# Kernel optimization log

Hardware: AMD Instinct MI355X
Metric: run time of the kernel (lower is better)

Reference implementation:

```python
import jax, jax.numpy as jnp
from jax import lax
import numpy as np

# Mamba2 config from PixelMamba.__init__
D_MODEL = 128; D_STATE = 256; D_CONV = 4; EXPAND = 4; HEADDIM = 32
D_INNER = EXPAND * D_MODEL              # 512
NHEADS = D_INNER // HEADDIM             # 16
NGROUPS = 1
D_XBC = D_INNER + 2 * NGROUPS * D_STATE # 1024 (conv channels)
D_IN_PROJ = 2 * D_INNER + 2 * NGROUPS * D_STATE + NHEADS  # 1552
CHUNK = 128                             # SSD chunk length


def setup_inputs() -> dict:
    key = jax.random.key(0)
    ks = jax.random.split(key, 10)
    Bb, C, H, W = 2, 3, 64, 64
    f32 = jnp.float32
    rn = lambda k, shape, s: jax.random.normal(k, shape, f32) * s
    return {
        "x": jax.random.normal(ks[0], (Bb, C, H, W), f32),
        "fc0_w": rn(ks[1], (3, D_MODEL), 1.0 / np.sqrt(3.0)),
        "fc0_b": rn(ks[2], (D_MODEL,), 0.01),
        "in_proj_w": rn(ks[3], (D_MODEL, D_IN_PROJ), 1.0 / np.sqrt(D_MODEL)),
        "conv_w": rn(ks[4], (D_XBC, D_CONV), 1.0 / np.sqrt(D_CONV)),
        "conv_b": rn(ks[5], (D_XBC,), 0.01),
        "dt_bias": jnp.log(jnp.expm1(jax.random.uniform(ks[6], (NHEADS,), f32, 0.001, 0.1))),
        "A_log": jnp.log(jax.random.uniform(ks[7], (NHEADS,), f32, 1.0, 16.0)),
        "D": rn(ks[8], (NHEADS,), 1.0),
        "norm_w": jnp.ones((D_INNER,), f32),
        "out_proj_w": rn(ks[9], (D_INNER, D_MODEL), 1.0 / np.sqrt(D_INNER)),
    }


def _mamba2(u, in_proj_w, conv_w, conv_b, dt_bias, A_log, D, norm_w, out_proj_w):
    # u: (B, L, d_model)
    Bb, L, _ = u.shape
    zxbcdt = u @ in_proj_w                                     # (B,L,1552)
    z = zxbcdt[..., :D_INNER]                                  # gate
    xBC = zxbcdt[..., D_INNER:D_INNER + D_XBC]
    dt = jax.nn.softplus(zxbcdt[..., -NHEADS:] + dt_bias)     # (B,L,H)

    # causal depthwise conv1d + SiLU
    xc = lax.conv_general_dilated(
        xBC.transpose(0, 2, 1), conv_w[:, None, :], (1,), [(D_CONV - 1, 0)],
        dimension_numbers=('NCH', 'OIH', 'NCH'), feature_group_count=D_XBC)
    xBC = jax.nn.silu(xc + conv_b[None, :, None]).transpose(0, 2, 1)

    xs = xBC[..., :D_INNER].reshape(Bb, L, NHEADS, HEADDIM)    # (B,L,H,P)
    Bm = xBC[..., D_INNER:D_INNER + D_STATE]                   # (B,L,N), ngroups=1
    Cm = xBC[..., D_INNER + D_STATE:]                          # (B,L,N)
    A = -jnp.exp(A_log)                                        # (H,) negative

    # ---- SSD chunked selective scan ----
    NC = L // CHUNK
    a = (dt * A).reshape(Bb, NC, CHUNK, NHEADS)                # log-decay per step (<=0)
    dt_r = dt.reshape(Bb, NC, CHUNK, NHEADS)
    x_r = xs.reshape(Bb, NC, CHUNK, NHEADS, HEADDIM)
    B_r = Bm.reshape(Bb, NC, CHUNK, D_STATE)
    C_r = Cm.reshape(Bb, NC, CHUNK, D_STATE)
    cum = jnp.cumsum(a, axis=2)                                # (B,NC,Q,H)

    # intra-chunk quadratic part: attn[t,s] = (C_t.B_s) * exp(cum_t - cum_s) * dt_s, s<=t
    mask = jnp.tril(jnp.ones((CHUNK, CHUNK), bool))
    diff = cum[:, :, :, None, :] - cum[:, :, None, :, :]       # (B,NC,t,s,H)
    decay = jnp.exp(jnp.where(mask[None, None, :, :, None], diff, -jnp.inf))
    CB = jnp.einsum('bctn,bcsn->bcts', C_r, B_r)
    attn = CB[..., None] * decay * dt_r[:, :, None, :, :]      # (B,NC,t,s,H)
    y_intra = jnp.einsum('bctsh,bcshp->bcthp', attn, x_r)

    # per-chunk end states: sum_s exp(cum_end - cum_s) dt_s x_s B_s^T
    decay_end = jnp.exp(cum[:, :, -1:, :] - cum)               # (B,NC,Q,H)
    states = jnp.einsum('bcsh,bcsn,bcshp->bchpn', decay_end * dt_r, B_r, x_r)

    # inter-chunk recurrence over NC chunks (small sequential scan)
    chunk_decay = jnp.exp(cum[:, :, -1, :])                    # (B,NC,H)
    def step(S, inp):
        cd, st = inp
        return S * cd[..., None, None] + st, S                 # emit state BEFORE chunk
    S0 = jnp.zeros((Bb, NHEADS, HEADDIM, D_STATE), u.dtype)
    _, prev = lax.scan(step, S0, (chunk_decay.transpose(1, 0, 2),
                                  states.transpose(1, 0, 2, 3, 4)))
    prev = prev.transpose(1, 0, 2, 3, 4)                       # (B,NC,H,P,N)
    y_inter = jnp.einsum('bcth,bctn,bchpn->bcthp', jnp.exp(cum), C_r, prev)

    y = (y_intra + y_inter).reshape(Bb, L, NHEADS, HEADDIM) + D[None, None, :, None] * xs
    y = y.reshape(Bb, L, D_INNER)

    # gated RMSNorm (norm_before_gate=False): norm(y * silu(z)) * w
    y = y * jax.nn.silu(z)
    y = y * lax.rsqrt(jnp.mean(y * y, axis=-1, keepdims=True) + 1e-5) * norm_w
    return y @ out_proj_w


def reference(x, fc0_w, fc0_b, in_proj_w, conv_w, conv_b, dt_bias, A_log, D, norm_w, out_proj_w):
    Bb, C, H, W = x.shape
    x1 = x.transpose(0, 2, 3, 1).reshape(Bb, -1, C)            # raster order
    x2 = x[:, :, ::-1, ::-1].transpose(0, 2, 3, 1).reshape(Bb, -1, C)  # flipped
    u = jnp.concatenate([x1, x2], axis=1) @ fc0_w + fc0_b      # (B, 2HW, 128)
    return _mamba2(u, in_proj_w, conv_w, conv_b, dt_bias, A_log, D, norm_w, out_proj_w)
```

## Files before the change

### kernel.cpp

```cpp
#include <hip/hip_runtime.h>

typedef short short8 __attribute__((ext_vector_type(8)));
typedef float f32x4 __attribute__((ext_vector_type(4)));
typedef unsigned short ushort;
typedef unsigned int uint;

#define MFMA16(a,b,c) __builtin_amdgcn_mfma_f32_16x16x32_bf16(a,b,c,0,0,0)
#define DPROJ 1552

constexpr size_t OFF_M    = 0;
constexpr size_t OFF_CB_B = 0x5000;
constexpr size_t OFF_WT   = 0x8000;
constexpr size_t OFF_XT   = 0x30000;
constexpr size_t OFF_DT   = OFF_XT  + 16777216ull;
constexpr size_t OFF_BCM  = OFF_DT  + 1048576ull;
constexpr size_t OFF_CUM  = OFF_BCM + 16777216ull;
constexpr size_t OFF_CDC  = OFF_CUM + 1048576ull;
constexpr size_t OFF_CBT  = OFF_CDC + 8192ull;
constexpr size_t OFF_BT   = OFF_CBT + 4194304ull;
constexpr size_t OFF_ST   = OFF_BT  + 8388608ull;
constexpr size_t OFF_Y    = OFF_ST  + 33554432ull;

__device__ __forceinline__ float sigm(float x){ return 1.0f/(1.0f + __expf(-x)); }
__device__ __forceinline__ ushort f2bf(float f){
  union { float f; uint u; } c; c.f = f;
  uint u = c.u;
  return (ushort)((u + 0x7FFFu + ((u>>16)&1u)) >> 16);
}
__device__ __forceinline__ float bf2f(ushort h){
  union { uint u; float f; } c; c.u = ((uint)h)<<16;
  return c.f;
}
__device__ __forceinline__ void swz2048(int p, int& bc, int& h){
  int xcd = p & 7, slot = p >> 3;
  bc = xcd*16 + (slot >> 4);
  h  = slot & 15;
}

__global__ __launch_bounds__(256) void k0_prep(const float* __restrict__ fc0_w,
                                               const float* __restrict__ fc0_b,
                                               const float* __restrict__ W,
                                               char* __restrict__ wsb){
  float* Mo = (float*)(wsb + OFF_M);
  float* Co = (float*)(wsb + OFF_CB_B);
  int j = blockIdx.x*256 + threadIdx.x;
  if (j >= DPROJ) return;
  float m0=0.f,m1=0.f,m2=0.f,cc=0.f;
  for (int d=0; d<128; ++d){
    float w = W[(size_t)d*DPROJ + j];
    m0 = fmaf(fc0_w[d],     w, m0);
    m1 = fmaf(fc0_w[128+d], w, m1);
    m2 = fmaf(fc0_w[256+d], w, m2);
    cc = fmaf(fc0_b[d],     w, cc);
  }
  Mo[j] = m0; Mo[DPROJ + j] = m1; Mo[2*DPROJ + j] = m2;
  Co[j] = cc;
}

__global__ __launch_bounds__(256) void k0b_wt(const float* __restrict__ norm_w,
                                              const float* __restrict__ Wout,
                                              char* __restrict__ wsb){
  ushort* WT = (ushort*)(wsb + OFF_WT);
  int d = blockIdx.x;
  for (int i = threadIdx.x; i < 512; i += 256)
    WT[(size_t)d*512 + i] = f2bf(norm_w[i]*Wout[(size_t)i*128 + d]);
}

__global__ __launch_bounds__(256) void k1dt(const float* __restrict__ x,
                                            const float* __restrict__ dt_bias,
                                            char* __restrict__ wsb){
  int idx = blockIdx.x*256 + threadIdx.x;
  int r = idx >> 4, hh = idx & 15;
  int b = r >> 13, l = r & 8191;
  int hp, wv;
  if (l < 4096){ hp = l>>6; wv = l&63; }
  else { int l2 = l-4096; hp = 63-(l2>>6); wv = 63-(l2&63); }
  const float* xb = x + (size_t)b*12288;
  float x0 = xb[hp*64+wv], x1 = xb[4096+hp*64+wv], x2 = xb[8192+hp*64+wv];
  const float* M  = (const float*)(wsb + OFF_M);
  const float* Cc = (const float*)(wsb + OFF_CB_B);
  int j = 1536 + hh;
  float v = Cc[j];
  v = fmaf(x0, M[j], v);
  v = fmaf(x1, M[DPROJ+j], v);
  v = fmaf(x2, M[2*DPROJ+j], v);
  float t = v + dt_bias[hh];
  ((float*)(wsb+OFF_DT))[(size_t)r*16+hh] = (t > 20.f) ? t : log1pf(__expf(t));
}

__device__ __forceinline__ void proj8(int li, const float* __restrict__ xb,
                                      const float* m0, const float* m1, const float* m2,
                                      const float* c8, float* dst){
  if (li < 0){
    #pragma unroll
    for (int j=0;j<8;++j) dst[j] = 0.f;
    return;
  }
  int hh, wv;
  if (li < 4096){ hh = li>>6; wv = li&63; }
  else { int l2 = li-4096; hh = 63-(l2>>6); wv = 63-(l2&63); }
  float x0 = xb[hh*64+wv], x1 = xb[4096+hh*64+wv], x2 = xb[8192+hh*64+wv];
  #pragma unroll
  for (int j=0;j<8;++j)
    dst[j] = fmaf(x2, m2[j], fmaf(x1, m1[j], fmaf(x0, m0[j], c8[j])));
}

__device__ __forceinline__ void conv8(const float* cb8, const float* cw0, const float* cw1,
                                      const float* cw2, const float* cw3,
                                      const float* wA, const float* wB,
                                      const float* wC, const float* wD, ushort* o){
  #pragma unroll
  for (int j=0;j<8;++j){
    float a = cb8[j];
    a = fmaf(wA[j], cw0[j], a);
    a = fmaf(wB[j], cw1[j], a);
    a = fmaf(wC[j], cw2[j], a);
    a = fmaf(wD[j], cw3[j], a);
    o[j] = f2bf(a * sigm(a));
  }
}
__device__ __forceinline__ void cp8(ushort* d, const ushort* s){
  #pragma unroll
  for (int j=0;j<8;++j) d[j] = s[j];
}

__global__ __launch_bounds__(256) void k12_projconv(const float* __restrict__ x,
                                                    const float* __restrict__ conv_w,
                                                    const float* __restrict__ conv_b,
                                                    char* __restrict__ wsb){
  int tid = threadIdx.x;
  int cg = tid & 127, rl = tid >> 7;
  int row0 = blockIdx.x*16 + rl*8;
  int b = row0 >> 13, l0 = row0 & 8191;
  const float* M  = (const float*)(wsb + OFF_M);
  const float* Cc = (const float*)(wsb + OFF_CB_B);
  const float* xb = x + (size_t)b*12288;
  int ch0 = cg*8, j0 = 512 + ch0;
  float m0[8],m1[8],m2[8],c8[8],cw0[8],cw1[8],cw2[8],cw3[8],cb8[8];
  #pragma unroll
  for (int j=0;j<8;++j){
    m0[j]=M[j0+j]; m1[j]=M[DPROJ+j0+j]; m2[j]=M[2*DPROJ+j0+j]; c8[j]=Cc[j0+j];
    cw0[j]=conv_w[(ch0+j)*4+0]; cw1[j]=conv_w[(ch0+j)*4+1];
    cw2[j]=conv_w[(ch0+j)*4+2]; cw3[j]=conv_w[(ch0+j)*4+3];
    cb8[j]=conv_b[ch0+j];
  }
  bool is_xs = (ch0 < 512);
  ushort* bcmp = (ushort*)(wsb + OFF_BCM);
  int chb = ch0 - 512;
  uint colw[8][4];
  ushort oprev[8];
  float w0[8],w1[8],w2[8],w3[8];
  ushort o[8];
  proj8(l0-3, xb, m0,m1,m2,c8, w1);
  proj8(l0-2, xb, m0,m1,m2,c8, w2);
  proj8(l0-1, xb, m0,m1,m2,c8, w3);

#define ROW_EVEN(R, WN, WA, WB, WC)                                          \
  proj8(l0+R, xb, m0,m1,m2,c8, WN);                                          \
  conv8(cb8,cw0,cw1,cw2,cw3, WA,WB,WC,WN, o);                                \
  if (is_xs) cp8(oprev, o);                                                  \
  else *(uint4*)(bcmp + (size_t)(row0+R)*512 + chb) = *(uint4*)o;
#define ROW_ODD(R, WN, WA, WB, WC)                                           \
  proj8(l0+R, xb, m0,m1,m2,c8, WN);                                          \
  conv8(cb8,cw0,cw1,cw2,cw3, WA,WB,WC,WN, o);                                \
  if (is_xs){ _Pragma("unroll")                                              \
    for (int j=0;j<8;++j) colw[j][(R)>>1] = (uint)oprev[j] | ((uint)o[j]<<16); } \
  else *(uint4*)(bcmp + (size_t)(row0+R)*512 + chb) = *(uint4*)o;

  ROW_EVEN(0, w0, w1,w2,w3)
  ROW_ODD (1, w1, w2,w3,w0)
  ROW_EVEN(2, w2, w3,w0,w1)
  ROW_ODD (3, w3, w0,w1,w2)
  ROW_EVEN(4, w0, w1,w2,w3)
  ROW_ODD (5, w1, w2,w3,w0)
  ROW_EVEN(6, w2, w3,w0,w1)
  ROW_ODD (7, w3, w0,w1,w2)
#undef ROW_EVEN
#undef ROW_ODD

  if (is_xs){
    int h = ch0>>5, p0 = ch0&31;
    int bc = row0>>7, grp = (row0&127)>>3;
    ushort* dst = (ushort*)(wsb+OFF_XT) + (((size_t)(bc*16+h)*16 + grp)*32)*8;
    #pragma unroll
    for (int j=0;j<8;++j){
      uint4 v; v.x = colw[j][0]; v.y = colw[j][1]; v.z = colw[j][2]; v.w = colw[j][3];
      *(uint4*)(dst + (size_t)(p0+j)*8) = v;
    }
  }
}

__global__ __launch_bounds__(128) void k3_cum(const float* __restrict__ A_log,
                                              char* __restrict__ wsb){
  int bi = blockIdx.x;
  int h = bi & 15;
  int t = threadIdx.x;
  __shared__ float s[128];
  float A = -__expf(A_log[h]);
  const float* dtp = (const float*)(wsb + OFF_DT);
  size_t row = (size_t)(bi>>4)*128 + t;
  float a = dtp[row*16 + h] * A;
  s[t] = a; __syncthreads();
  for (int off=1; off<128; off<<=1){
    float v = (t>=off) ? s[t-off] : 0.f;
    __syncthreads();
    s[t] += v;
    __syncthreads();
  }
  ((float*)(wsb + OFF_CUM))[(size_t)bi*128 + t] = s[t];
  if (t==127) ((float*)(wsb + OFF_CDC))[bi] = __expf(s[127]);
}

__global__ __launch_bounds__(256) void k4a_cb(char* __restrict__ wsb){
  int bi = blockIdx.x;
  int sq = bi & 3; int bc = bi >> 2;
  __shared__ __align__(16) char sC[16384];
  __shared__ __align__(16) char sB[4096];
  const ushort* bcm = (const ushort*)(wsb + OFF_BCM);
  ushort* cbtT = (ushort*)(wsb + OFF_CBT) + (size_t)bc*16384;
  size_t rb = (size_t)bc*128;
  int tid = threadIdx.x;
  int lane = tid&63, wid = tid>>6, l15 = lane&15, l4 = lane>>4;
  int s_base = sq*32;
  f32x4 acc[2][2] = {};
  for (int nt = 0; nt < 4; ++nt){
    int n0 = nt*64;
    __syncthreads();
    for (int idx = tid; idx < 1024; idx += 256){
      int t = idx>>3, c = idx&7;
      uint4 v = *(const uint4*)(bcm + (rb+t)*512 + 256 + n0 + c*8);
      *(uint4*)(sC + ((t*128 + c*16) ^ ((t&7)<<4))) = v;
    }
    {
      int idx = tid;
      int s = idx>>3, c = idx&7;
      uint4 v = *(const uint4*)(bcm + (rb+s_base+s)*512 + n0 + c*8);
      *(uint4*)(sB + ((s*128 + c*16) ^ ((s&7)<<4))) = v;
    }
    __syncthreads();
    #pragma unroll
    for (int ks = 0; ks < 2; ++ks){
      int kb = ks*64 + l4*16;
      int t0 = wid*32 + l15, t1 = t0 + 16;
      short8 a0 = *(const short8*)(sC + ((t0*128 + kb) ^ ((t0&7)<<4)));
      short8 a1 = *(const short8*)(sC + ((t1*128 + kb) ^ ((t1&7)<<4)));
      short8 b0 = *(const short8*)(sB + ((l15*128 + kb) ^ ((l15&7)<<4)));
      short8 b1 = *(const short8*)(sB + (((16+l15)*128 + kb) ^ (((16+l15)&7)<<4)));
      acc[0][0] = MFMA16(a0,b0,acc[0][0]);
      acc[0][1] = MFMA16(a0,b1,acc[0][1]);
      acc[1][0] = MFMA16(a1,b0,acc[1][0]);
      acc[1][1] = MFMA16(a1,b1,acc[1][1]);
    }
  }
  #pragma unroll
  for (int mt=0; mt<2; ++mt)
  #pragma unroll
  for (int st=0; st<2; ++st)
  #pragma unroll
  for (int r=0; r<4; ++r){
    int t = wid*32 + mt*16 + l4*4 + r;
    int s = s_base + st*16 + l15;
    cbtT[(size_t)((s>>3)*128 + t)*8 + (s&7)] = f2bf(acc[mt][st][r]);
  }
}

__global__ __launch_bounds__(256) void k4t_bt(char* __restrict__ wsb){
  int bc = blockIdx.x; int n = threadIdx.x;
  const ushort* bcm = (const ushort*)(wsb + OFF_BCM);
  size_t rb = (size_t)bc*128;
  uint pk[64];
  #pragma unroll
  for (int s2 = 0; s2 < 64; ++s2){
    uint lo = bcm[(rb + 2*s2  )*512 + n];
    uint hi = bcm[(rb + 2*s2+1)*512 + n];
    pk[s2] = lo | (hi<<16);
  }
  ushort* btb = (ushort*)(wsb + OFF_BT) + (size_t)bc*32768;
  #pragma unroll
  for (int grp=0; grp<16; ++grp){
    uint4 v; v.x = pk[grp*4]; v.y = pk[grp*4+1]; v.z = pk[grp*4+2]; v.w = pk[grp*4+3];
    *(uint4*)(btb + (size_t)(grp*256 + n)*8) = v;
  }
}

__global__ __launch_bounds__(256) void k4s_states(char* __restrict__ wsb){
  int bc, h; swz2048(blockIdx.x, bc, h);
  int bi = bc*16 + h;
  __shared__ float sW[128];
  const ushort* xt  = (const ushort*)(wsb + OFF_XT) + (size_t)bi*4096;
  const ushort* btb = (const ushort*)(wsb + OFF_BT) + (size_t)bc*32768;
  const float* cum  = (const float*)(wsb + OFF_CUM) + (size_t)bi*128;
  const float* dtp  = (const float*)(wsb + OFF_DT);
  ushort* st = (ushort*)(wsb + OFF_ST) + (size_t)bi*8192;
  size_t rb = (size_t)bc*128;
  int tid = threadIdx.x;
  if (tid < 128){
    float c127 = cum[127];
    sW[tid] = __expf(c127 - cum[tid]) * dtp[(rb+tid)*16 + h];
  }
  __syncthreads();
  int lane = tid&63, wid = tid>>6, l15 = lane&15, l4 = lane>>4;
  f32x4 acc2[2][4] = {};
  #pragma unroll
  for (int ks = 0; ks < 4; ++ks){
    int grp = ks*4 + l4;
    const float* wp = sW + grp*8;
    short8 ra0 = *(const short8*)(xt + (size_t)(grp*32 + l15)*8);
    short8 ra1 = *(const short8*)(xt + (size_t)(grp*32 + 16 + l15)*8);
    short8 a0, a1;
    #pragma unroll
    for (int j=0;j<8;++j){
      a0[j] = (short)f2bf(bf2f((ushort)ra0[j]) * wp[j]);
      a1[j] = (short)f2bf(bf2f((ushort)ra1[j]) * wp[j]);
    }
    #pragma unroll
    for (int ntl = 0; ntl < 4; ++ntl){
      int n = wid*64 + ntl*16 + l15;
      short8 b = *(const short8*)(btb + (size_t)(grp*256 + n)*8);
      acc2[0][ntl] = MFMA16(a0,b,acc2[0][ntl]);
      acc2[1][ntl] = MFMA16(a1,b,acc2[1][ntl]);
    }
  }
  #pragma unroll
  for (int mt=0; mt<2; ++mt)
  #pragma unroll
  for (int ntl=0; ntl<4; ++ntl)
  #pragma unroll
  for (int r=0; r<4; ++r){
    int p = mt*16 + l4*4 + r;
    int n = wid*64 + ntl*16 + l15;
    st[(size_t)((n>>3)*32 + p)*8 + (n&7)] = f2bf(acc2[mt][ntl][r]);
  }
}

__global__ __launch_bounds__(256) void k5_scan(char* __restrict__ wsb){
  int g = blockIdx.x*256 + threadIdx.x;
  int l = g & 63;
  int e = l & 7, plow = l >> 3;
  int up = g >> 6;
  int p = (up & 3)*8 + plow; up >>= 2;
  int grp = up & 31; up >>= 5;
  int h = up & 15; int b = up >> 4;
  int off = (grp*32 + p)*8 + e;
  ushort* st = (ushort*)(wsb + OFF_ST);
  const float* cdc = (const float*)(wsb + OFF_CDC);
  float S = 0.f;
  for (int c=0; c<64; ++c){
    int bi = (b*64+c)*16 + h;
    size_t idx = (size_t)bi*8192 + off;
    float v = bf2f(st[idx]);
    st[idx] = f2bf(S);
    S = fmaf(S, cdc[bi], v);
  }
}

__global__ __launch_bounds__(256) void k4y_out(const float* __restrict__ Dp,
                                               char* __restrict__ wsb){
  int bc, h; swz2048(blockIdx.x, bc, h);
  int bi = bc*16 + h;
  __shared__ float sCum[128], sDt[128], sE[128];
  const ushort* cbt = (const ushort*)(wsb + OFF_CBT) + (size_t)bc*16384;
  const ushort* xt  = (const ushort*)(wsb + OFF_XT) + (size_t)bi*4096;
  const ushort* bcm = (const ushort*)(wsb + OFF_BCM);
  const ushort* prev= (const ushort*)(wsb + OFF_ST) + (size_t)bi*8192;
  const float* cum  = (const float*)(wsb + OFF_CUM) + (size_t)bi*128;
  const float* dtp  = (const float*)(wsb + OFF_DT);
  float* Y = (float*)(wsb + OFF_Y);
  size_t rb = (size_t)bc*128;
  int tid = threadIdx.x;
  if (tid < 128){
    float cv = cum[tid];
    sCum[tid] = cv;
    sDt[tid]  = dtp[(rb+tid)*16 + h];
    sE[tid]   = __expf(cv);
  }
  __syncthreads();
  int lane = tid&63, wid = tid>>6, l15 = lane&15, l4 = lane>>4;
  int t0 = wid*32 + l15, t1 = t0 + 16;
  float ct0 = sCum[t0], ct1 = sCum[t1];
  f32x4 acc[2][2] = {};
  #pragma unroll
  for (int ks = 0; ks < 4; ++ks){
    int grp = ks*4 + l4;
    int s0 = grp*8;
    short8 ra0 = *(const short8*)(cbt + (size_t)(grp*128 + t0)*8);
    short8 ra1 = *(const short8*)(cbt + (size_t)(grp*128 + t1)*8);
    short8 a0, a1;
    #pragma unroll
    for (int j=0;j<8;++j){
      int s = s0 + j;
      float cs = sCum[s], ds = sDt[s];
      float e0 = __expf(fminf(ct0 - cs, 0.f)) * ds;
      float e1 = __expf(fminf(ct1 - cs, 0.f)) * ds;
      float v0 = (t0 >= s) ? bf2f((ushort)ra0[j]) * e0 : 0.f;
      float v1 = (t1 >= s) ? bf2f((ushort)ra1[j]) * e1 : 0.f;
      a0[j] = (short)f2bf(v0);
      a1[j] = (short)f2bf(v1);
    }
    short8 b0 = *(const short8*)(xt + (size_t)(grp*32 + l15)*8);
    short8 b1 = *(const short8*)(xt + (size_t)(grp*32 + 16 + l15)*8);
    acc[0][0] = MFMA16(a0,b0,acc[0][0]);
    acc[0][1] = MFMA16(a0,b1,acc[0][1]);
    acc[1][0] = MFMA16(a1,b0,acc[1][0]);
    acc[1][1] = MFMA16(a1,b1,acc[1][1]);
  }
  f32x4 acc2[2][2] = {};
  #pragma unroll
  for (int ks = 0; ks < 8; ++ks){
    int koff = ks*32 + l4*8;
    int grp = ks*4 + l4;
    short8 a0 = *(const short8*)(bcm + (rb+t0)*512 + 256 + koff);
    short8 a1 = *(const short8*)(bcm + (rb+t1)*512 + 256 + koff);
    short8 b0 = *(const short8*)(prev + (size_t)(grp*32 + l15)*8);
    short8 b1 = *(const short8*)(prev + (size_t)(grp*32 + 16 + l15)*8);
    acc2[0][0] = MFMA16(a0,b0,acc2[0][0]);
    acc2[0][1] = MFMA16(a0,b1,acc2[0][1]);
    acc2[1][0] = MFMA16(a1,b0,acc2[1][0]);
    acc2[1][1] = MFMA16(a1,b1,acc2[1][1]);
  }
  float Dh = Dp[h];
  #pragma unroll
  for (int mt=0; mt<2; ++mt){
    int tb = wid*32 + mt*16 + l4*4;
    int tg = tb>>3, e0 = tb&7;
    #pragma unroll
    for (int nt=0; nt<2; ++nt){
      int p = nt*16 + l15;
      ushort xv[4];
      *(uint2*)xv = *(const uint2*)(xt + (size_t)(tg*32 + p)*8 + e0);
      #pragma unroll
      for (int r=0; r<4; ++r){
        int t = tb + r;
        Y[(rb+t)*512 + h*32 + p] = acc[mt][nt][r] + sE[t]*acc2[mt][nt][r] + Dh*bf2f(xv[r]);
      }
    }
  }
}

__global__ __launch_bounds__(256) void k7_final(const float* __restrict__ x,
                                                char* __restrict__ wsb,
                                                float* __restrict__ out){
  int r0 = blockIdx.x*32;
  __shared__ __align__(16) char sG[32768];
  __shared__ float sScale[32];
  const float* Y  = (const float*)(wsb + OFF_Y);
  const float* M  = (const float*)(wsb + OFF_M);
  const float* Cb = (const float*)(wsb + OFF_CB_B);
  const ushort* WT = (const ushort*)(wsb + OFF_WT);
  int tid = threadIdx.x;
  int r = tid>>3, li = tid&7;
  int row = r0 + r; int b = row>>13, l = row & 8191;
  int hh, wv;
  if (l < 4096){ hh = l>>6; wv = l&63; }
  else { int l2 = l-4096; hh = 63-(l2>>6); wv = 63-(l2&63); }
  const float* xb = x + (size_t)b*12288;
  float x0 = xb[hh*64+wv], x1 = xb[4096+hh*64+wv], x2 = xb[8192+hh*64+wv];
  float sq = 0.f;
  for (int k = 0; k < 64; ++k){
    int i = li + 8*k;
    float z = Cb[i];
    z = fmaf(x0, M[i], z);
    z = fmaf(x1, M[DPROJ+i], z);
    z = fmaf(x2, M[2*DPROJ+i], z);
    float y = Y[(size_t)row*512 + i];
    float g = y * z * sigm(z);
    sq = fmaf(g, g, sq);
    *(ushort*)(sG + ((r*1024 + i*2) ^ ((r&7)<<4))) = f2bf(g);
  }
  sq += __shfl_xor(sq, 1, 64);
  sq += __shfl_xor(sq, 2, 64);
  sq += __shfl_xor(sq, 4, 64);
  if (li == 0) sScale[r] = rsqrtf(sq*(1.f/512.f) + 1e-5f);
  __syncthreads();
  int lane = tid&63, wid = tid>>6, l15 = lane&15, l4 = lane>>4;
  f32x4 acc[2][2] = {};
  #pragma unroll
  for (int ks = 0; ks < 16; ++ks){
    int kb = ks*64 + l4*16;
    int rr0 = l15, rr1 = 16+l15;
    short8 a0 = *(const short8*)(sG + ((rr0*1024 + kb) ^ ((rr0&7)<<4)));
    short8 a1 = *(const short8*)(sG + ((rr1*1024 + kb) ^ ((rr1&7)<<4)));
    int koff = ks*32 + l4*8;
    short8 b0 = *(const short8*)(WT + (size_t)(wid*32 + l15)*512 + koff);
    short8 b1 = *(const short8*)(WT + (size_t)(wid*32 + 16 + l15)*512 + koff);
    acc[0][0] = MFMA16(a0,b0,acc[0][0]);
    acc[0][1] = MFMA16(a0,b1,acc[0][1]);
    acc[1][0] = MFMA16(a1,b0,acc[1][0]);
    acc[1][1] = MFMA16(a1,b1,acc[1][1]);
  }
  #pragma unroll
  for (int mt=0; mt<2; ++mt)
  #pragma unroll
  for (int nt=0; nt<2; ++nt)
  #pragma unroll
  for (int r4=0; r4<4; ++r4){
    int rr = mt*16 + l4*4 + r4;
    int d = wid*32 + nt*16 + l15;
    out[(size_t)(r0+rr)*128 + d] = acc[mt][nt][r4] * sScale[rr];
  }
}

extern "C" void kernel_launch(void* const* d_in, const int* in_sizes, int n_in,
                              void* d_out, int out_size, void* d_ws, size_t ws_size,
                              hipStream_t stream) {
  const float* x         = (const float*)d_in[0];
  const float* fc0_w     = (const float*)d_in[1];
  const float* fc0_b     = (const float*)d_in[2];
  const float* in_proj_w = (const float*)d_in[3];
  const float* conv_w    = (const float*)d_in[4];
  const float* conv_b    = (const float*)d_in[5];
  const float* dt_bias   = (const float*)d_in[6];
  const float* A_log     = (const float*)d_in[7];
  const float* Dp        = (const float*)d_in[8];
  const float* norm_w    = (const float*)d_in[9];
  const float* out_proj_w= (const float*)d_in[10];
  char* wsb  = (char*)d_ws;
  float* out = (float*)d_out;

  k0_prep<<<dim3(7),     dim3(256), 0, stream>>>(fc0_w, fc0_b, in_proj_w, wsb);
  k0b_wt <<<dim3(128),   dim3(256), 0, stream>>>(norm_w, out_proj_w, wsb);
  k1dt   <<<dim3(1024),  dim3(256), 0, stream>>>(x, dt_bias, wsb);
  k12_projconv<<<dim3(1024), dim3(256), 0, stream>>>(x, conv_w, conv_b, wsb);
  k3_cum <<<dim3(2048),  dim3(128), 0, stream>>>(A_log, wsb);
  k4a_cb <<<dim3(512),   dim3(256), 0, stream>>>(wsb);
  k4t_bt <<<dim3(128),   dim3(256), 0, stream>>>(wsb);
  k4s_states<<<dim3(2048), dim3(256), 0, stream>>>(wsb);
  k5_scan<<<dim3(1024),  dim3(256), 0, stream>>>(wsb);
  k4y_out<<<dim3(2048),  dim3(256), 0, stream>>>(Dp, wsb);
  k7_final<<<dim3(512),  dim3(256), 0, stream>>>(x, wsb, out);
}
```

Before: 155.0 us.

## Fuse dt into cumsum, B-transpose into CB kernel, store Y as bf16

The dt softplus computation moves into the cumulative-sum kernel, and the B-transpose kernel is folded into the CB matmul kernel, which reuses the B tile it already stages in shared memory. This removes two launches and a global round-trip of dt and B. The intermediate Y is now written as bf16 instead of fp32 and read back with vectorised 16-byte loads in the final kernel, halving that traffic. The trade-off is a small precision loss on Y before the gated RMSNorm.

```diff
diff --git a/kernel.cpp b/kernel.cpp
--- a/kernel.cpp
+++ b/kernel.cpp
@@ -66,28 +66,6 @@
     WT[(size_t)d*512 + i] = f2bf(norm_w[i]*Wout[(size_t)i*128 + d]);
 }
 
-__global__ __launch_bounds__(256) void k1dt(const float* __restrict__ x,
-                                            const float* __restrict__ dt_bias,
-                                            char* __restrict__ wsb){
-  int idx = blockIdx.x*256 + threadIdx.x;
-  int r = idx >> 4, hh = idx & 15;
-  int b = r >> 13, l = r & 8191;
-  int hp, wv;
-  if (l < 4096){ hp = l>>6; wv = l&63; }
-  else { int l2 = l-4096; hp = 63-(l2>>6); wv = 63-(l2&63); }
-  const float* xb = x + (size_t)b*12288;
-  float x0 = xb[hp*64+wv], x1 = xb[4096+hp*64+wv], x2 = xb[8192+hp*64+wv];
-  const float* M  = (const float*)(wsb + OFF_M);
-  const float* Cc = (const float*)(wsb + OFF_CB_B);
-  int j = 1536 + hh;
-  float v = Cc[j];
-  v = fmaf(x0, M[j], v);
-  v = fmaf(x1, M[DPROJ+j], v);
-  v = fmaf(x2, M[2*DPROJ+j], v);
-  float t = v + dt_bias[hh];
-  ((float*)(wsb+OFF_DT))[(size_t)r*16+hh] = (t > 20.f) ? t : log1pf(__expf(t));
-}
-
 __device__ __forceinline__ void proj8(int li, const float* __restrict__ xb,
                                       const float* m0, const float* m1, const float* m2,
                                       const float* c8, float* dst){
@@ -190,21 +168,37 @@
   }
 }
 
-__global__ __launch_bounds__(128) void k3_cum(const float* __restrict__ A_log,
+__global__ __launch_bounds__(128) void k3_cum(const float* __restrict__ x,
+                                              const float* __restrict__ dt_bias,
+                                              const float* __restrict__ A_log,
                                               char* __restrict__ wsb){
   int bi = blockIdx.x;
-  int h = bi & 15;
+  int h = bi & 15; int bc = bi >> 4;
   int t = threadIdx.x;
+  int r = bc*128 + t;
+  int b = r >> 13, l = r & 8191;
+  int hp, wv;
+  if (l < 4096){ hp = l>>6; wv = l&63; }
+  else { int l2 = l-4096; hp = 63-(l2>>6); wv = 63-(l2&63); }
+  const float* xb = x + (size_t)b*12288;
+  float x0 = xb[hp*64+wv], x1 = xb[4096+hp*64+wv], x2 = xb[8192+hp*64+wv];
+  const float* M  = (const float*)(wsb + OFF_M);
+  const float* Cc = (const float*)(wsb + OFF_CB_B);
+  int j = 1536 + h;
+  float v = Cc[j];
+  v = fmaf(x0, M[j], v);
+  v = fmaf(x1, M[DPROJ+j], v);
+  v = fmaf(x2, M[2*DPROJ+j], v);
+  float tt = v + dt_bias[h];
+  float dtv = (tt > 20.f) ? tt : log1pf(__expf(tt));
+  ((float*)(wsb+OFF_DT))[(size_t)r*16 + h] = dtv;
   __shared__ float s[128];
   float A = -__expf(A_log[h]);
-  const float* dtp = (const float*)(wsb + OFF_DT);
-  size_t row = (size_t)(bi>>4)*128 + t;
-  float a = dtp[row*16 + h] * A;
-  s[t] = a; __syncthreads();
+  s[t] = dtv * A; __syncthreads();
   for (int off=1; off<128; off<<=1){
-    float v = (t>=off) ? s[t-off] : 0.f;
+    float sv = (t>=off) ? s[t-off] : 0.f;
     __syncthreads();
-    s[t] += v;
+    s[t] += sv;
     __syncthreads();
   }
   ((float*)(wsb + OFF_CUM))[(size_t)bi*128 + t] = s[t];
@@ -218,6 +212,7 @@
   __shared__ __align__(16) char sB[4096];
   const ushort* bcm = (const ushort*)(wsb + OFF_BCM);
   ushort* cbtT = (ushort*)(wsb + OFF_CBT) + (size_t)bc*16384;
+  ushort* btb  = (ushort*)(wsb + OFF_BT)  + (size_t)bc*32768;
   size_t rb = (size_t)bc*128;
   int tid = threadIdx.x;
   int lane = tid&63, wid = tid>>6, l15 = lane&15, l4 = lane>>4;
@@ -238,6 +233,16 @@
       *(uint4*)(sB + ((s*128 + c*16) ^ ((s&7)<<4))) = v;
     }
     __syncthreads();
+    {
+      int grp_l = tid>>6, n_l = tid&63;
+      ushort o[8];
+      #pragma unroll
+      for (int sj=0; sj<8; ++sj){
+        int sl = grp_l*8 + sj;
+        o[sj] = *(const ushort*)(sB + ((sl*128 + n_l*2) ^ ((sl&7)<<4)));
+      }
+      *(uint4*)(btb + (size_t)((sq*4+grp_l)*256 + n0 + n_l)*8) = *(uint4*)o;
+    }
     #pragma unroll
     for (int ks = 0; ks < 2; ++ks){
       int kb = ks*64 + l4*16;
@@ -261,25 +266,6 @@
     int t = wid*32 + mt*16 + l4*4 + r;
     int s = s_base + st*16 + l15;
     cbtT[(size_t)((s>>3)*128 + t)*8 + (s&7)] = f2bf(acc[mt][st][r]);
-  }
-}
-
-__global__ __launch_bounds__(256) void k4t_bt(char* __restrict__ wsb){
-  int bc = blockIdx.x; int n = threadIdx.x;
-  const ushort* bcm = (const ushort*)(wsb + OFF_BCM);
-  size_t rb = (size_t)bc*128;
-  uint pk[64];
-  #pragma unroll
-  for (int s2 = 0; s2 < 64; ++s2){
-    uint lo = bcm[(rb + 2*s2  )*512 + n];
-    uint hi = bcm[(rb + 2*s2+1)*512 + n];
-    pk[s2] = lo | (hi<<16);
-  }
-  ushort* btb = (ushort*)(wsb + OFF_BT) + (size_t)bc*32768;
-  #pragma unroll
-  for (int grp=0; grp<16; ++grp){
-    uint4 v; v.x = pk[grp*4]; v.y = pk[grp*4+1]; v.z = pk[grp*4+2]; v.w = pk[grp*4+3];
-    *(uint4*)(btb + (size_t)(grp*256 + n)*8) = v;
   }
 }
 
@@ -365,7 +351,7 @@
   const ushort* prev= (const ushort*)(wsb + OFF_ST) + (size_t)bi*8192;
   const float* cum  = (const float*)(wsb + OFF_CUM) + (size_t)bi*128;
   const float* dtp  = (const float*)(wsb + OFF_DT);
-  float* Y = (float*)(wsb + OFF_Y);
+  ushort* Yb = (ushort*)(wsb + OFF_Y);
   size_t rb = (size_t)bc*128;
   int tid = threadIdx.x;
   if (tid < 128){
@@ -431,7 +417,8 @@
       #pragma unroll
       for (int r=0; r<4; ++r){
         int t = tb + r;
-        Y[(rb+t)*512 + h*32 + p] = acc[mt][nt][r] + sE[t]*acc2[mt][nt][r] + Dh*bf2f(xv[r]);
+        float yv = acc[mt][nt][r] + sE[t]*acc2[mt][nt][r] + Dh*bf2f(xv[r]);
+        Yb[(rb+t)*512 + h*32 + p] = f2bf(yv);
       }
     }
   }
@@ -443,7 +430,7 @@
   int r0 = blockIdx.x*32;
   __shared__ __align__(16) char sG[32768];
   __shared__ float sScale[32];
-  const float* Y  = (const float*)(wsb + OFF_Y);
+  const ushort* Yb = (const ushort*)(wsb + OFF_Y);
   const float* M  = (const float*)(wsb + OFF_M);
   const float* Cb = (const float*)(wsb + OFF_CB_B);
   const ushort* WT = (const ushort*)(wsb + OFF_WT);
@@ -456,16 +443,23 @@
   const float* xb = x + (size_t)b*12288;
   float x0 = xb[hh*64+wv], x1 = xb[4096+hh*64+wv], x2 = xb[8192+hh*64+wv];
   float sq = 0.f;
-  for (int k = 0; k < 64; ++k){
-    int i = li + 8*k;
-    float z = Cb[i];
-    z = fmaf(x0, M[i], z);
-    z = fmaf(x1, M[DPROJ+i], z);
-    z = fmaf(x2, M[2*DPROJ+i], z);
-    float y = Y[(size_t)row*512 + i];
-    float g = y * z * sigm(z);
-    sq = fmaf(g, g, sq);
-    *(ushort*)(sG + ((r*1024 + i*2) ^ ((r&7)<<4))) = f2bf(g);
+  #pragma unroll
+  for (int k = 0; k < 8; ++k){
+    int i0 = li*64 + k*8;
+    short8 yv = *(const short8*)(Yb + (size_t)row*512 + i0);
+    ushort g8[8];
+    #pragma unroll
+    for (int j=0;j<8;++j){
+      int i = i0 + j;
+      float z = Cb[i];
+      z = fmaf(x0, M[i], z);
+      z = fmaf(x1, M[DPROJ+i], z);
+      z = fmaf(x2, M[2*DPROJ+i], z);
+      float g = bf2f((ushort)yv[j]) * z * sigm(z);
+      sq = fmaf(g, g, sq);
+      g8[j] = f2bf(g);
+    }
+    *(uint4*)(sG + ((r*1024 + i0*2) ^ ((r&7)<<4))) = *(uint4*)g8;
   }
   sq += __shfl_xor(sq, 1, 64);
   sq += __shfl_xor(sq, 2, 64);
@@ -519,11 +513,9 @@
 
   k0_prep<<<dim3(7),     dim3(256), 0, stream>>>(fc0_w, fc0_b, in_proj_w, wsb);
   k0b_wt <<<dim3(128),   dim3(256), 0, stream>>>(norm_w, out_proj_w, wsb);
-  k1dt   <<<dim3(1024),  dim3(256), 0, stream>>>(x, dt_bias, wsb);
   k12_projconv<<<dim3(1024), dim3(256), 0, stream>>>(x, conv_w, conv_b, wsb);
-  k3_cum <<<dim3(2048),  dim3(128), 0, stream>>>(A_log, wsb);
+  k3_cum <<<dim3(2048),  dim3(128), 0, stream>>>(x, dt_bias, A_log, wsb);
   k4a_cb <<<dim3(512),   dim3(256), 0, stream>>>(wsb);
-  k4t_bt <<<dim3(128),   dim3(256), 0, stream>>>(wsb);
   k4s_states<<<dim3(2048), dim3(256), 0, stream>>>(wsb);
   k5_scan<<<dim3(1024),  dim3(256), 0, stream>>>(wsb);
   k4y_out<<<dim3(2048),  dim3(256), 0, stream>>>(Dp, wsb);
```

Measured after the change: 152.8 us. No clear change (-1.4%).
